# Kernel optimization log

Hardware: AMD Instinct MI355X
Metric: run time of the kernel (lower is better)

Reference implementation:

```python
import jax, jax.numpy as jnp
import numpy as np

B, L, D_MODEL = 2, 4096, 768
D_STATE, D_CONV, EXPAND = 16, 4, 2
D_INNER = EXPAND * D_MODEL
DT_RANK = -(-D_MODEL // 16)  # ceil(d_model/16) = 48


def _silu(x):
    return x * jax.nn.sigmoid(x)


def _dwconv(x, w, b):
    # x: (B, D_INNER, L); w: (D_INNER, K). Causal depthwise conv (torch pads both
    # sides with K-1 then slices [:L] == left-pad K-1, right-pad 0).
    y = jax.lax.conv_general_dilated(
        x, w[:, None, :], window_strides=(1,), padding=[(w.shape[-1] - 1, 0)],
        dimension_numbers=('NCH', 'OIH', 'NCH'), feature_group_count=x.shape[1])
    return y + b[None, :, None]


def _selective_scan(u, delta, A, Bm, Cm, Dv):
    # u, delta: (b,d,L); A: (d,n); Bm, Cm: (b,n,L); Dv: (d,)
    uT = jnp.moveaxis(u, -1, 0)      # (L,b,d)
    dT = jnp.moveaxis(delta, -1, 0)  # (L,b,d)
    BT = jnp.moveaxis(Bm, -1, 0)     # (L,b,n)
    CT = jnp.moveaxis(Cm, -1, 0)     # (L,b,n)

    def step(h, inp):
        u_t, d_t, B_t, C_t = inp
        dA = jnp.exp(d_t[..., None] * A)                       # (b,d,n)
        h = dA * h + (d_t * u_t)[..., None] * B_t[:, None, :]  # (b,d,n)
        y = jnp.einsum('bdn,bn->bd', h, C_t)
        return h, y

    h0 = jnp.zeros((u.shape[0], A.shape[0], A.shape[1]), u.dtype)
    _, ys = jax.lax.scan(step, h0, (uT, dT, BT, CT))
    y = jnp.moveaxis(ys, 0, -1)  # (b,d,L)
    return y + u * Dv[None, :, None]


def _branch(x, z, conv_w, conv_b, xproj_w, dtproj_w, dt_bias, A_log, Dv):
    x = _silu(_dwconv(x, conv_w, conv_b))
    dbl = jnp.einsum('bdl,ed->bel', x, xproj_w)  # e = DT_RANK + 2*D_STATE
    dt_low = dbl[:, :DT_RANK]
    Bm = dbl[:, DT_RANK:DT_RANK + D_STATE]
    Cm = dbl[:, DT_RANK + D_STATE:]
    dt = jnp.einsum('brl,dr->bdl', dt_low, dtproj_w)
    delta = jax.nn.softplus(dt + dt_bias[None, :, None])
    A = -jnp.exp(A_log)
    y = _selective_scan(x, delta, A, Bm, Cm, Dv)
    return y * _silu(z)


def _forward(hidden_states, in_proj_w, out_proj_w, conv_w_a, conv_b_a, conv_w_b,
             conv_b_b, x_proj_a_w, x_proj_b_w, dt_proj_a_w, dt_proj_b_w,
             dt_bias_a, dt_bias_b, A_a_log, A_b_log, D_a, D_b):
    xz = jnp.einsum('bld,ed->bel', hidden_states, in_proj_w)  # (B, 2*D_INNER, L)
    x_a, z_a = xz[:, :D_INNER], xz[:, D_INNER:]
    y_a = _branch(x_a, z_a, conv_w_a, conv_b_a, x_proj_a_w, dt_proj_a_w,
                  dt_bias_a, A_a_log, D_a)
    xz_b = xz[:, :, ::-1]  # flip sequence for backward direction
    x_b, z_b = xz_b[:, :D_INNER], xz_b[:, D_INNER:]
    y_b = _branch(x_b, z_b, conv_w_b, conv_b_b, x_proj_b_w, dt_proj_b_w,
                  dt_bias_b, A_b_log, D_b)
    y = y_a + y_b[:, :, ::-1]
    return jnp.einsum('bdl,od->blo', y, out_proj_w)  # (B, L, D_MODEL)


def setup_inputs() -> dict:
    key = jax.random.key(0)
    ks = jax.random.split(key, 10)
    s = 0.02
    rng = np.random.default_rng(0)
    # dt bias init: inverse-softplus of dt ~ LogUniform(1e-3, 1e-1)
    dt = np.exp(rng.uniform(size=D_INNER) * (np.log(0.1) - np.log(0.001))
                + np.log(0.001)).clip(min=1e-4)
    inv_dt = (dt + np.log(-np.expm1(-dt))).astype(np.float32)
    A_log = np.log(np.tile(np.arange(1, D_STATE + 1, dtype=np.float32),
                           (D_INNER, 1)))
    return {
        'hidden_states': jax.random.normal(ks[0], (B, L, D_MODEL), jnp.float32),
        'in_proj_w': s * jax.random.normal(ks[1], (2 * D_INNER, D_MODEL), jnp.float32),
        'out_proj_w': s * jax.random.normal(ks[2], (D_MODEL, D_INNER), jnp.float32),
        'conv_w_a': s * jax.random.normal(ks[3], (D_INNER, D_CONV), jnp.float32),
        'conv_b_a': jnp.zeros((D_INNER,), jnp.float32),
        'conv_w_b': s * jax.random.normal(ks[4], (D_INNER, D_CONV), jnp.float32),
        'conv_b_b': jnp.zeros((D_INNER,), jnp.float32),
        'x_proj_a_w': s * jax.random.normal(ks[5], (DT_RANK + 2 * D_STATE, D_INNER), jnp.float32),
        'x_proj_b_w': s * jax.random.normal(ks[6], (DT_RANK + 2 * D_STATE, D_INNER), jnp.float32),
        'dt_proj_a_w': (DT_RANK ** -0.5) * jax.random.uniform(ks[7], (D_INNER, DT_RANK), jnp.float32, -1.0, 1.0),
        'dt_proj_b_w': (DT_RANK ** -0.5) * jax.random.uniform(ks[8], (D_INNER, DT_RANK), jnp.float32, -1.0, 1.0),
        'dt_bias_a': jnp.asarray(inv_dt),
        'dt_bias_b': jnp.asarray(inv_dt),
        'A_a_log': jnp.asarray(A_log),
        'A_b_log': jnp.asarray(A_log),
        'D_a': jnp.ones((D_INNER,), jnp.float32),
        'D_b': jnp.ones((D_INNER,), jnp.float32),
    }


def reference(hidden_states, in_proj_w, out_proj_w, conv_w_a, conv_b_a, conv_w_b,
              conv_b_b, x_proj_a_w, x_proj_b_w, dt_proj_a_w, dt_proj_b_w,
              dt_bias_a, dt_bias_b, A_a_log, A_b_log, D_a, D_b):
    return _forward(hidden_states, in_proj_w, out_proj_w, conv_w_a, conv_b_a,
                    conv_w_b, conv_b_b, x_proj_a_w, x_proj_b_w, dt_proj_a_w,
                    dt_proj_b_w, dt_bias_a, dt_bias_b, A_a_log, A_b_log, D_a, D_b)
```

## Files before the change

### kernel.cpp

```cpp
#include <hip/hip_runtime.h>
#include <math.h>

#define BQ 2
#define LQ 4096
#define DM 768
#define DI 1536
#define DS 16
#define E80 80
#define NC 32
#define CH 128

typedef _Float16 half8 __attribute__((ext_vector_type(8)));
typedef _Float16 half4v __attribute__((ext_vector_type(4)));
typedef float f32x4 __attribute__((ext_vector_type(4)));

__device__ __forceinline__ ushort f2h_bits(float x) {
    return __builtin_bit_cast(ushort, (_Float16)x);
}

#define GLDS16(gsrc, ldst)                                                  \
    __builtin_amdgcn_global_load_lds(                                       \
        (const __attribute__((address_space(1))) void*)(gsrc),              \
        (__attribute__((address_space(3))) void*)(ldst), 16, 0, 0)

__global__ __launch_bounds__(256)
void pack_fp16(const float* __restrict__ src, _Float16* __restrict__ dst)
{
    long i = ((long)blockIdx.x * 256 + threadIdx.x) * 4;
    float4 v = *(const float4*)(src + i);
    half4v o = {(_Float16)v.x, (_Float16)v.y, (_Float16)v.z, (_Float16)v.w};
    *(half4v*)(dst + i) = o;
}

__global__ __launch_bounds__(256)
void pack_dtw(const float* __restrict__ dwa, const float* __restrict__ dwb,
              _Float16* __restrict__ dtw)
{
    int idx = blockIdx.x * 256 + threadIdx.x;
    int br = idx / DI, d = idx % DI;
    const float* W = (br ? dwb : dwa) + (long)d * 48;
    _Float16* o = dtw + (long)idx * 64;
#pragma unroll
    for (int k = 0; k < 48; k++) o[k] = (_Float16)W[k];
#pragma unroll
    for (int k = 48; k < 64; k++) o[k] = (_Float16)0.f;
}

template <typename CT>
__global__ __launch_bounds__(256, 4)
void gemm_mfma(const _Float16* __restrict__ Ah, const _Float16* __restrict__ Bh,
               CT* __restrict__ C, int K, int ldA, int ldB, int ldC,
               long strideA, long strideB, long strideC)
{
    __shared__ uint4 Af[2][16][64];
    __shared__ uint4 Bf[2][16][64];
    const int bz = blockIdx.z;
    const _Float16* Ab = Ah + (long)bz * strideA;
    const _Float16* Bb = Bh + (long)bz * strideB;
    CT* Cb = C + (long)bz * strideC;
    const int m0 = blockIdx.y * 128, n0 = blockIdx.x * 128;
    const int tid = threadIdx.x, w = tid >> 6, lane = tid & 63;
    const int mh = w & 1, nh = w >> 1;

    const _Float16* asrc[4];
    const _Float16* bsrc[4];
#pragma unroll
    for (int i = 0; i < 4; i++) {
        int f = w * 4 + i;
        int ks = f >> 3, t = f & 7;
        asrc[i] = Ab + (long)(m0 + t * 16 + (lane & 15)) * ldA + ks * 32 + (lane >> 4) * 8;
        bsrc[i] = Bb + (long)(n0 + t * 16 + (lane & 15)) * ldB + ks * 32 + (lane >> 4) * 8;
    }

    f32x4 acc[4][4];
#pragma unroll
    for (int i = 0; i < 4; i++)
#pragma unroll
        for (int j = 0; j < 4; j++) acc[i][j] = {0.f, 0.f, 0.f, 0.f};

    const int nt = K >> 6;

#pragma unroll
    for (int i = 0; i < 4; i++) {
        GLDS16(asrc[i], &Af[0][w * 4 + i][0]);
        GLDS16(bsrc[i], &Bf[0][w * 4 + i][0]);
        asrc[i] += 64; bsrc[i] += 64;
    }
    if (nt > 1) {
#pragma unroll
        for (int i = 0; i < 4; i++) {
            GLDS16(asrc[i], &Af[1][w * 4 + i][0]);
            GLDS16(bsrc[i], &Bf[1][w * 4 + i][0]);
            asrc[i] += 64; bsrc[i] += 64;
        }
    }

    for (int t = 0; t < nt; ++t) {
        const int cur = t & 1;
        if (t + 1 < nt)
            asm volatile("s_waitcnt vmcnt(8)" ::: "memory");
        else
            asm volatile("s_waitcnt vmcnt(0)" ::: "memory");
        __builtin_amdgcn_s_barrier();

#pragma unroll
        for (int ks = 0; ks < 2; ks++) {
            uint4 bu[4];
#pragma unroll
            for (int j = 0; j < 4; j++)
                bu[j] = Bf[cur][ks * 8 + nh * 4 + j][lane];
#pragma unroll
            for (int i = 0; i < 4; i++) {
                uint4 au = Af[cur][ks * 8 + mh * 4 + i][lane];
                half8 av = __builtin_bit_cast(half8, au);
#pragma unroll
                for (int j = 0; j < 4; j++) {
                    half8 bv = __builtin_bit_cast(half8, bu[j]);
                    acc[i][j] = __builtin_amdgcn_mfma_f32_16x16x32_f16(
                        av, bv, acc[i][j], 0, 0, 0);
                }
            }
        }
        __builtin_amdgcn_s_barrier();

        if (t + 2 < nt) {
#pragma unroll
            for (int i = 0; i < 4; i++) {
                GLDS16(asrc[i], &Af[cur][w * 4 + i][0]);
                GLDS16(bsrc[i], &Bf[cur][w * 4 + i][0]);
                asrc[i] += 64; bsrc[i] += 64;
            }
        }
    }

    const int r0 = (lane >> 4) * 4, cn = lane & 15;
#pragma unroll
    for (int i = 0; i < 4; i++) {
        int mrow = m0 + (mh * 4 + i) * 16 + r0;
#pragma unroll
        for (int j = 0; j < 4; j++) {
            int col = n0 + (nh * 4 + j) * 16 + cn;
#pragma unroll
            for (int r = 0; r < 4; r++)
                Cb[(long)(mrow + r) * ldC + col] = (CT)acc[i][j][r];
        }
    }
}

__global__ __launch_bounds__(256)
void conv_silu_t(const _Float16* __restrict__ xz,
                 const float* __restrict__ cwa, const float* __restrict__ cba,
                 const float* __restrict__ cwb, const float* __restrict__ cbb,
                 _Float16* __restrict__ ut)
{
    __shared__ float lraw[64][67];
    __shared__ float cu[64][72];
    __shared__ float lcw[64][5];
    const int l0 = blockIdx.x * 64, d0 = blockIdx.y * 64;
    const int z = blockIdx.z;
    const int br = z >> 1, b = z & 1;
    const _Float16* xb = xz + ((long)b * 2 * DI + d0) * LQ;
    const float* CW = br ? cwb : cwa;
    const float* CB = br ? cbb : cba;
    const int tid = threadIdx.x;

    {
        int dd = tid >> 2, k = tid & 3;
        lcw[dd][k] = CW[(d0 + dd) * 4 + k];
        if (tid < 64) lcw[tid][4] = CB[d0 + tid];
    }
    for (int i = tid; i < 64 * 67; i += 256) {
        int dd = i / 67, cc = i % 67;
        int src = l0 - 3 + cc;
        float v = 0.f;
        if (src >= 0)
            v = (float)xb[(long)dd * LQ + (br ? (LQ - 1 - src) : src)];
        lraw[dd][cc] = v;
    }
    __syncthreads();
#pragma unroll
    for (int q = 0; q < 16; q++) {
        int o = tid + q * 256;
        int dd = o & 63, ll = o >> 6;
        float a = lcw[dd][4];
        a = fmaf(lraw[dd][ll + 0], lcw[dd][0], a);
        a = fmaf(lraw[dd][ll + 1], lcw[dd][1], a);
        a = fmaf(lraw[dd][ll + 2], lcw[dd][2], a);
        a = fmaf(lraw[dd][ll + 3], lcw[dd][3], a);
        cu[ll][dd] = a * (1.f / (1.f + __expf(-a)));
    }
    __syncthreads();
    const int dg = (tid & 7) * 8;
#pragma unroll
    for (int p = 0; p < 2; p++) {
        int ll = (tid >> 3) + p * 32;
        float4 v0 = *(const float4*)&cu[ll][dg];
        float4 v1 = *(const float4*)&cu[ll][dg + 4];
        uint4 o;
        o.x = f2h_bits(v0.x) | ((unsigned)f2h_bits(v0.y) << 16);
        o.y = f2h_bits(v0.z) | ((unsigned)f2h_bits(v0.w) << 16);
        o.z = f2h_bits(v1.x) | ((unsigned)f2h_bits(v1.y) << 16);
        o.w = f2h_bits(v1.z) | ((unsigned)f2h_bits(v1.w) << 16);
        *(uint4*)(ut + ((long)z * LQ + l0 + ll) * DI + d0 + dg) = o;
    }
}

__global__ __launch_bounds__(256)
void xproj_mfma(const _Float16* __restrict__ ut, const _Float16* __restrict__ xpw,
                float* __restrict__ dbl)
{
    __shared__ uint4 Af[8][64];
    __shared__ uint4 Bf[10][64];
    const int m0 = blockIdx.x * 64;
    const int z = blockIdx.y;
    const _Float16* A = ut + (long)z * LQ * DI;
    const _Float16* W = xpw + (long)(z >> 1) * E80 * DI;
    float* out = dbl + (long)z * LQ * E80;
    const int tid = threadIdx.x, w = tid >> 6, lane = tid & 63;

    f32x4 acc[5];
#pragma unroll
    for (int j = 0; j < 5; j++) acc[j] = {0.f, 0.f, 0.f, 0.f};

    for (int k0 = 0; k0 < DI; k0 += 64) {
#pragma unroll
        for (int i = 0; i < 2; i++) {
            int f = w + i * 4;
            int row = m0 + (f & 3) * 16 + (lane & 15);
            int koff = k0 + (f >> 2) * 32 + (lane >> 4) * 8;
            Af[f][lane] = *(const uint4*)(A + (long)row * DI + koff);
        }
        for (int i = tid; i < 640; i += 256) {
            int f = i >> 6, ln = i & 63;
            int e = (f >> 1) * 16 + (ln & 15);
            int koff = k0 + (f & 1) * 32 + (ln >> 4) * 8;
            Bf[f][ln] = *(const uint4*)(W + (long)e * DI + koff);
        }
        __syncthreads();
#pragma unroll
        for (int ks = 0; ks < 2; ks++) {
            half8 av = __builtin_bit_cast(half8, Af[ks * 4 + w][lane]);
#pragma unroll
            for (int j = 0; j < 5; j++) {
                half8 bv = __builtin_bit_cast(half8, Bf[j * 2 + ks][lane]);
                acc[j] = __builtin_amdgcn_mfma_f32_16x16x32_f16(av, bv, acc[j], 0, 0, 0);
            }
        }
        __syncthreads();
    }
    const int r0 = (lane >> 4) * 4, cn = lane & 15;
    const int row = m0 + w * 16 + r0;
#pragma unroll
    for (int j = 0; j < 5; j++)
#pragma unroll
        for (int r = 0; r < 4; r++)
            out[(long)(row + r) * E80 + j * 16 + cn] = acc[j][r];
}

__global__ __launch_bounds__(256)
void delta_mfma(const float* __restrict__ dbl, const _Float16* __restrict__ dtw,
                const float* __restrict__ dba, const float* __restrict__ dbb,
                _Float16* __restrict__ dlt)
{
    __shared__ uint4 Af[8][64];
    __shared__ uint4 Bf[16][64];
    const int m0 = blockIdx.x * 64;
    const int n0 = blockIdx.y * 128;
    const int z  = blockIdx.z;
    const float* bias = (z >> 1) ? dbb : dba;
    const float* Ab = dbl + (long)z * LQ * E80;
    const _Float16* Wb = dtw + (long)(z >> 1) * DI * 64;
    _Float16* ob = dlt + (long)z * LQ * DI;
    const int tid = threadIdx.x, w = tid >> 6, lane = tid & 63;

#pragma unroll
    for (int i = 0; i < 2; i++) {
        int s = tid + i * 256;
        int f = s >> 6, ln = s & 63;
        int mt = f >> 1, ks = f & 1;
        int row = m0 + mt * 16 + (ln & 15);
        int koff = ks * 32 + (ln >> 4) * 8;
        uint4 o = {0u, 0u, 0u, 0u};
        if (koff < 48) {
            const float* p = Ab + (long)row * E80 + koff;
            float4 v0 = *(const float4*)p;
            float4 v1 = *(const float4*)(p + 4);
            o.x = f2h_bits(v0.x) | ((unsigned)f2h_bits(v0.y) << 16);
            o.y = f2h_bits(v0.z) | ((unsigned)f2h_bits(v0.w) << 16);
            o.z = f2h_bits(v1.x) | ((unsigned)f2h_bits(v1.y) << 16);
            o.w = f2h_bits(v1.z) | ((unsigned)f2h_bits(v1.w) << 16);
        }
        Af[f][ln] = o;
    }
#pragma unroll
    for (int i = 0; i < 4; i++) {
        int s = tid + i * 256;
        int f = s >> 6, ln = s & 63;
        int nt = f >> 1, ks = f & 1;
        int d = n0 + nt * 16 + (ln & 15);
        int koff = ks * 32 + (ln >> 4) * 8;
        Bf[f][ln] = *(const uint4*)(Wb + (long)d * 64 + koff);
    }
    __syncthreads();

    f32x4 acc[8];
#pragma unroll
    for (int j = 0; j < 8; j++) acc[j] = {0.f, 0.f, 0.f, 0.f};
#pragma unroll
    for (int ks = 0; ks < 2; ks++) {
        half8 av = __builtin_bit_cast(half8, Af[w * 2 + ks][lane]);
#pragma unroll
        for (int j = 0; j < 8; j++) {
            half8 bv = __builtin_bit_cast(half8, Bf[j * 2 + ks][lane]);
            acc[j] = __builtin_amdgcn_mfma_f32_16x16x32_f16(av, bv, acc[j], 0, 0, 0);
        }
    }
    const int r0 = (lane >> 4) * 4, cn = lane & 15;
    const int row = m0 + w * 16 + r0;
#pragma unroll
    for (int j = 0; j < 8; j++) {
        int d = n0 + j * 16 + cn;
        float bi = bias[d];
#pragma unroll
        for (int r = 0; r < 4; r++) {
            float a = acc[j][r] + bi;
            float sp = (a > 20.f) ? a : __logf(1.f + __expf(a));
            ob[(long)(row + r) * DI + d] = (_Float16)sp;
        }
    }
}

__global__ __launch_bounds__(256)
void transpose_z(const _Float16* __restrict__ xz, _Float16* __restrict__ zt)
{
    __shared__ float t[64][65];
    const int l0 = blockIdx.x * 64, d0 = blockIdx.y * 64, b = blockIdx.z;
    const _Float16* src = xz + ((long)b * 2 * DI + DI + d0) * LQ + l0;
    const int tid = threadIdx.x;
#pragma unroll
    for (int p = 0; p < 2; p++) {
        int g = tid + p * 256;
        int dd = g >> 3, c8 = (g & 7) * 8;
        half8 v = *(const half8*)&src[(long)dd * LQ + c8];
#pragma unroll
        for (int j = 0; j < 8; j++) t[c8 + j][dd] = (float)v[j];
    }
    __syncthreads();
    const int l = tid >> 2, seg = (tid & 3) * 16;
    ushort tmp[16];
#pragma unroll
    for (int j = 0; j < 16; j++) tmp[j] = f2h_bits(t[l][seg + j]);
    uint4 p0, p1;
    p0.x = tmp[0] | (tmp[1] << 16);  p0.y = tmp[2] | (tmp[3] << 16);
    p0.z = tmp[4] | (tmp[5] << 16);  p0.w = tmp[6] | (tmp[7] << 16);
    p1.x = tmp[8] | (tmp[9] << 16);  p1.y = tmp[10] | (tmp[11] << 16);
    p1.z = tmp[12] | (tmp[13] << 16); p1.w = tmp[14] | (tmp[15] << 16);
    ushort* dst = (ushort*)(zt + ((long)b * LQ + l0 + l) * DI + d0 + seg);
    *(uint4*)dst = p0;
    *(uint4*)(dst + 8) = p1;
}

__global__ __launch_bounds__(256)
void scan_p1(const _Float16* __restrict__ ut, const _Float16* __restrict__ dlt,
             const float* __restrict__ dbl,
             const float* __restrict__ Ala, const float* __restrict__ Alb,
             float* __restrict__ Sdl, float* __restrict__ Hloc)
{
    const int d = blockIdx.x * 256 + threadIdx.x;
    const int c = blockIdx.y;
    const int z = blockIdx.z;
    const int br = z >> 1;
    const float* Al = br ? Alb : Ala;
    float An[16];
#pragma unroll
    for (int i = 0; i < 4; i++) {
        float4 v = *(const float4*)&Al[(long)d * 16 + i * 4];
        An[i * 4] = -__expf(v.x); An[i * 4 + 1] = -__expf(v.y);
        An[i * 4 + 2] = -__expf(v.z); An[i * 4 + 3] = -__expf(v.w);
    }
    bool fast = true;
#pragma unroll
    for (int n = 0; n < 16; n++)
        fast = fast && (__builtin_fabsf(An[n] + (float)(n + 1)) < 1e-3f);

    const long lbase = (long)z * LQ + (long)c * CH;
    const _Float16* ub = ut + lbase * DI + d;
    const _Float16* db = dlt + lbase * DI + d;
    const float* bc = dbl + lbase * E80 + 48;

    float h[16];
#pragma unroll
    for (int n = 0; n < 16; n++) h[n] = 0.f;
    float sdl = 0.f;

    for (int t0 = 0; t0 < CH; t0 += 8) {
        _Float16 uu[8], dd[8];
#pragma unroll
        for (int j = 0; j < 8; j++) {
            uu[j] = ub[(long)(t0 + j) * DI];
            dd[j] = db[(long)(t0 + j) * DI];
        }
#pragma unroll
        for (int j = 0; j < 8; j++) {
            float dl = (float)dd[j];
            float u  = (float)uu[j];
            sdl += dl;
            float du = dl * u;
            const float* Bp = bc + (long)(t0 + j) * E80;
            float Bv[16];
#pragma unroll
            for (int i = 0; i < 4; i++) {
                float4 v = *(const float4*)&Bp[i * 4];
                Bv[i * 4] = v.x; Bv[i * 4 + 1] = v.y;
                Bv[i * 4 + 2] = v.z; Bv[i * 4 + 3] = v.w;
            }
            if (fast) {
                float r = __expf(-dl);
                float p = r;
                h[0] = fmaf(p, h[0], du * Bv[0]);
#pragma unroll
                for (int n = 1; n < 16; n++) {
                    p *= r;
                    h[n] = fmaf(p, h[n], du * Bv[n]);
                }
            } else {
#pragma unroll
                for (int n = 0; n < 16; n++)
                    h[n] = fmaf(__expf(dl * An[n]), h[n], du * Bv[n]);
            }
        }
    }
    Sdl[((long)z * NC + c) * DI + d] = sdl;
    float* Hp = Hloc + (((long)z * NC + c) * DI + d) * 16;
#pragma unroll
    for (int i = 0; i < 4; i++)
        *(float4*)&Hp[i * 4] = make_float4(h[i * 4], h[i * 4 + 1], h[i * 4 + 2], h[i * 4 + 3]);
}

__global__ __launch_bounds__(256)
void scan_p2(const float* __restrict__ Sdl, const float* __restrict__ Hloc,
             const float* __restrict__ Ala, const float* __restrict__ Alb,
             float* __restrict__ h0)
{
    const int idx = blockIdx.x * 256 + threadIdx.x;
    const int z = blockIdx.y;
    const int d = idx >> 4, n = idx & 15;
    const float* Al = (z >> 1) ? Alb : Ala;
    const float An = -__expf(Al[(long)d * 16 + n]);
    float h = 0.f;
    for (int c = 0; c < NC; c++) {
        h0[((long)z * NC + c) * DI * 16 + idx] = h;
        float sdl = Sdl[((long)z * NC + c) * DI + d];
        float Hl = Hloc[((long)z * NC + c) * DI * 16 + idx];
        h = fmaf(__expf(An * sdl), h, Hl);
    }
}

__global__ __launch_bounds__(256)
void scan_p3(const _Float16* __restrict__ ut, const _Float16* __restrict__ dlt,
             const float* __restrict__ dbl, const float* __restrict__ h0,
             const float* __restrict__ Ala, const float* __restrict__ Alb,
             const float* __restrict__ Da, const float* __restrict__ Db,
             _Float16* __restrict__ ya, _Float16* __restrict__ yb)
{
    const int d = blockIdx.x * 256 + threadIdx.x;
    const int c = blockIdx.y;
    const int z = blockIdx.z;
    const int br = z >> 1, b = z & 1;
    const float* Al = br ? Alb : Ala;
    float An[16];
#pragma unroll
    for (int i = 0; i < 4; i++) {
        float4 v = *(const float4*)&Al[(long)d * 16 + i * 4];
        An[i * 4] = -__expf(v.x); An[i * 4 + 1] = -__expf(v.y);
        An[i * 4 + 2] = -__expf(v.z); An[i * 4 + 3] = -__expf(v.w);
    }
    bool fast = true;
#pragma unroll
    for (int n = 0; n < 16; n++)
        fast = fast && (__builtin_fabsf(An[n] + (float)(n + 1)) < 1e-3f);

    const float Dd = (br ? Db : Da)[d];
    const long lbase = (long)z * LQ + (long)c * CH;
    const _Float16* ub = ut + lbase * DI + d;
    const _Float16* db = dlt + lbase * DI + d;
    const float* bc = dbl + lbase * E80 + 48;
    const float* Hp = h0 + (((long)z * NC + c) * DI + d) * 16;
    float h[16];
#pragma unroll
    for (int i = 0; i < 4; i++) {
        float4 v = *(const float4*)&Hp[i * 4];
        h[i * 4] = v.x; h[i * 4 + 1] = v.y; h[i * 4 + 2] = v.z; h[i * 4 + 3] = v.w;
    }
    _Float16* yo = br ? yb : ya;

    for (int t0 = 0; t0 < CH; t0 += 8) {
        _Float16 uu[8], dd[8];
#pragma unroll
        for (int j = 0; j < 8; j++) {
            uu[j] = ub[(long)(t0 + j) * DI];
            dd[j] = db[(long)(t0 + j) * DI];
        }
#pragma unroll
        for (int j = 0; j < 8; j++) {
            float dl = (float)dd[j];
            float u  = (float)uu[j];
            float du = dl * u;
            const float* Bp = bc + (long)(t0 + j) * E80;
            float Bv[16], Cv[16];
#pragma unroll
            for (int i = 0; i < 4; i++) {
                float4 v = *(const float4*)&Bp[i * 4];
                Bv[i * 4] = v.x; Bv[i * 4 + 1] = v.y;
                Bv[i * 4 + 2] = v.z; Bv[i * 4 + 3] = v.w;
                float4 w2 = *(const float4*)&Bp[16 + i * 4];
                Cv[i * 4] = w2.x; Cv[i * 4 + 1] = w2.y;
                Cv[i * 4 + 2] = w2.z; Cv[i * 4 + 3] = w2.w;
            }
            float y = u * Dd;
            if (fast) {
                float r = __expf(-dl);
                float p = r;
                h[0] = fmaf(p, h[0], du * Bv[0]);
                y = fmaf(h[0], Cv[0], y);
#pragma unroll
                for (int n = 1; n < 16; n++) {
                    p *= r;
                    h[n] = fmaf(p, h[n], du * Bv[n]);
                    y = fmaf(h[n], Cv[n], y);
                }
            } else {
#pragma unroll
                for (int n = 0; n < 16; n++) {
                    h[n] = fmaf(__expf(dl * An[n]), h[n], du * Bv[n]);
                    y = fmaf(h[n], Cv[n], y);
                }
            }
            int t = c * CH + t0 + j;
            long lorig = br ? (LQ - 1 - t) : t;
            yo[((long)b * LQ + lorig) * DI + d] = (_Float16)y;
        }
    }
}

__global__ __launch_bounds__(256)
void fuse_y(const _Float16* __restrict__ ya, const _Float16* __restrict__ yb,
            const _Float16* __restrict__ zt, _Float16* __restrict__ yf)
{
    long i = ((long)blockIdx.x * 256 + threadIdx.x) * 8;
    half8 a = *(const half8*)(ya + i);
    half8 b = *(const half8*)(yb + i);
    half8 zz = *(const half8*)(zt + i);
    half8 o;
#pragma unroll
    for (int j = 0; j < 8; j++) {
        float y = (float)a[j] + (float)b[j];
        float zv = (float)zz[j];
        o[j] = (_Float16)(y * (zv / (1.f + __expf(-zv))));
    }
    *(half8*)(yf + i) = o;
}

extern "C" void kernel_launch(void* const* d_in, const int* in_sizes, int n_in,
                              void* d_out, int out_size, void* d_ws, size_t ws_size,
                              hipStream_t stream)
{
    const float* hs  = (const float*)d_in[0];
    const float* Wi  = (const float*)d_in[1];
    const float* Wo  = (const float*)d_in[2];
    const float* cwa = (const float*)d_in[3];
    const float* cba = (const float*)d_in[4];
    const float* cwb = (const float*)d_in[5];
    const float* cbb = (const float*)d_in[6];
    const float* xpa = (const float*)d_in[7];
    const float* xpb = (const float*)d_in[8];
    const float* dwa = (const float*)d_in[9];
    const float* dwb = (const float*)d_in[10];
    const float* dba = (const float*)d_in[11];
    const float* dbb = (const float*)d_in[12];
    const float* Ala = (const float*)d_in[13];
    const float* Alb = (const float*)d_in[14];
    const float* Da  = (const float*)d_in[15];
    const float* Db  = (const float*)d_in[16];
    float* out = (float*)d_out;

    float* ws = (float*)d_ws;
    _Float16* xz   = (_Float16*)ws;
    _Float16* dl_t = (_Float16*)ws;
    _Float16* ya   = (_Float16*)(ws + 12582912);
    _Float16* yb   = (_Float16*)(ws + 18874368);
    float*    dbl  = ws + 25165824;
    _Float16* u_t  = (_Float16*)(ws + 26476544);
    _Float16* yf   = (_Float16*)(ws + 26476544);
    _Float16* z_t  = (_Float16*)(ws + 39059456);
    float*    Sdl  = ws + 45350912;
    float*    Hloc = ws + 45547520;
    float*    h0   = ws + 48693248;
    _Float16* hsb  = (_Float16*)(ws + 45350912);
    _Float16* Wib  = (_Float16*)(ws + 48496640);
    _Float16* xpw  = (_Float16*)(ws + 49676288);
    _Float16* dtw  = (_Float16*)(ws + 49799168);
    _Float16* Wob  = (_Float16*)(ws + 45350912);

    pack_fp16<<<6144, 256, 0, stream>>>(hs, hsb);
    pack_fp16<<<2304, 256, 0, stream>>>(Wi, Wib);
    pack_fp16<<<120, 256, 0, stream>>>(xpa, xpw);
    pack_fp16<<<120, 256, 0, stream>>>(xpb, xpw + 122880);
    pack_dtw<<<12, 256, 0, stream>>>(dwa, dwb, dtw);
    gemm_mfma<_Float16><<<dim3(32, 24, 2), 256, 0, stream>>>(
        Wib, hsb, xz, DM, DM, DM, LQ,
        0L, (long)LQ * DM, (long)2 * DI * LQ);
    conv_silu_t<<<dim3(64, 24, 4), 256, 0, stream>>>(xz, cwa, cba, cwb, cbb, u_t);
    xproj_mfma<<<dim3(64, 4), 256, 0, stream>>>(u_t, xpw, dbl);
    transpose_z<<<dim3(64, 24, 2), 256, 0, stream>>>(xz, z_t);
    delta_mfma<<<dim3(64, 12, 4), 256, 0, stream>>>(dbl, dtw, dba, dbb, dl_t);
    scan_p1<<<dim3(6, NC, 4), 256, 0, stream>>>(u_t, dl_t, dbl, Ala, Alb, Sdl, Hloc);
    scan_p2<<<dim3(96, 4), 256, 0, stream>>>(Sdl, Hloc, Ala, Alb, h0);
    scan_p3<<<dim3(6, NC, 4), 256, 0, stream>>>(u_t, dl_t, dbl, h0, Ala, Alb, Da, Db, ya, yb);
    pack_fp16<<<1152, 256, 0, stream>>>(Wo, Wob);
    fuse_y<<<6144, 256, 0, stream>>>(ya, yb, z_t, yf);
    gemm_mfma<float><<<dim3(6, 32, 2), 256, 0, stream>>>(
        yf, Wob, out, DI, DI, DI, DM,
        (long)LQ * DI, 0L, (long)LQ * DM);
}
```

Measured before the change: 551.2 us.

## Split-K the x_proj and out_proj GEMMs with atomic accumulation

Partitions the K dimension of the x_proj GEMM into four chunks and of the output projection GEMM into two, launching more blocks and accumulating partial results with float atomicAdd. Output buffers are zeroed with memsets beforehand. The aim is to fill more compute units on GEMMs whose grids were small (256 and 384 blocks). In exchange it adds atomic traffic, two memset operations and non-deterministic summation order.

```diff
diff --git a/kernel.cpp b/kernel.cpp
--- a/kernel.cpp
+++ b/kernel.cpp
@@ -46,18 +46,19 @@
     for (int k = 48; k < 64; k++) o[k] = (_Float16)0.f;
 }
 
-template <typename CT>
+template <typename CT, bool ATOMIC>
 __global__ __launch_bounds__(256, 4)
 void gemm_mfma(const _Float16* __restrict__ Ah, const _Float16* __restrict__ Bh,
                CT* __restrict__ C, int K, int ldA, int ldB, int ldC,
-               long strideA, long strideB, long strideC)
+               long strideA, long strideB, long strideC, int nbz, int koff)
 {
     __shared__ uint4 Af[2][16][64];
     __shared__ uint4 Bf[2][16][64];
     const int bz = blockIdx.z;
-    const _Float16* Ab = Ah + (long)bz * strideA;
-    const _Float16* Bb = Bh + (long)bz * strideB;
-    CT* Cb = C + (long)bz * strideC;
+    const int batch = bz % nbz, kh = bz / nbz;
+    const _Float16* Ab = Ah + (long)batch * strideA + (long)kh * koff;
+    const _Float16* Bb = Bh + (long)batch * strideB + (long)kh * koff;
+    CT* Cb = C + (long)batch * strideC;
     const int m0 = blockIdx.y * 128, n0 = blockIdx.x * 128;
     const int tid = threadIdx.x, w = tid >> 6, lane = tid & 63;
     const int mh = w & 1, nh = w >> 1;
@@ -141,8 +142,12 @@
         for (int j = 0; j < 4; j++) {
             int col = n0 + (nh * 4 + j) * 16 + cn;
 #pragma unroll
-            for (int r = 0; r < 4; r++)
-                Cb[(long)(mrow + r) * ldC + col] = (CT)acc[i][j][r];
+            for (int r = 0; r < 4; r++) {
+                if constexpr (ATOMIC)
+                    atomicAdd(&Cb[(long)(mrow + r) * ldC + col], acc[i][j][r]);
+                else
+                    Cb[(long)(mrow + r) * ldC + col] = (CT)acc[i][j][r];
+            }
         }
     }
 }
@@ -213,6 +218,7 @@
     __shared__ uint4 Bf[10][64];
     const int m0 = blockIdx.x * 64;
     const int z = blockIdx.y;
+    const int kh = blockIdx.z;
     const _Float16* A = ut + (long)z * LQ * DI;
     const _Float16* W = xpw + (long)(z >> 1) * E80 * DI;
     float* out = dbl + (long)z * LQ * E80;
@@ -222,7 +228,7 @@
 #pragma unroll
     for (int j = 0; j < 5; j++) acc[j] = {0.f, 0.f, 0.f, 0.f};
 
-    for (int k0 = 0; k0 < DI; k0 += 64) {
+    for (int k0 = kh * 384; k0 < (kh + 1) * 384; k0 += 64) {
 #pragma unroll
         for (int i = 0; i < 2; i++) {
             int f = w + i * 4;
@@ -254,7 +260,7 @@
     for (int j = 0; j < 5; j++)
 #pragma unroll
         for (int r = 0; r < 4; r++)
-            out[(long)(row + r) * E80 + j * 16 + cn] = acc[j][r];
+            atomicAdd(&out[(long)(row + r) * E80 + j * 16 + cn], acc[j][r]);
 }
 
 __global__ __launch_bounds__(256)
@@ -602,16 +608,18 @@
     _Float16* dtw  = (_Float16*)(ws + 49799168);
     _Float16* Wob  = (_Float16*)(ws + 45350912);
 
+    hipMemsetAsync(dbl, 0, (size_t)4 * LQ * E80 * sizeof(float), stream);
+    hipMemsetAsync(out, 0, (size_t)out_size, stream);
     pack_fp16<<<6144, 256, 0, stream>>>(hs, hsb);
     pack_fp16<<<2304, 256, 0, stream>>>(Wi, Wib);
     pack_fp16<<<120, 256, 0, stream>>>(xpa, xpw);
     pack_fp16<<<120, 256, 0, stream>>>(xpb, xpw + 122880);
     pack_dtw<<<12, 256, 0, stream>>>(dwa, dwb, dtw);
-    gemm_mfma<_Float16><<<dim3(32, 24, 2), 256, 0, stream>>>(
+    gemm_mfma<_Float16, false><<<dim3(32, 24, 2), 256, 0, stream>>>(
         Wib, hsb, xz, DM, DM, DM, LQ,
-        0L, (long)LQ * DM, (long)2 * DI * LQ);
+        0L, (long)LQ * DM, (long)2 * DI * LQ, 2, 0);
     conv_silu_t<<<dim3(64, 24, 4), 256, 0, stream>>>(xz, cwa, cba, cwb, cbb, u_t);
-    xproj_mfma<<<dim3(64, 4), 256, 0, stream>>>(u_t, xpw, dbl);
+    xproj_mfma<<<dim3(64, 4, 4), 256, 0, stream>>>(u_t, xpw, dbl);
     transpose_z<<<dim3(64, 24, 2), 256, 0, stream>>>(xz, z_t);
     delta_mfma<<<dim3(64, 12, 4), 256, 0, stream>>>(dbl, dtw, dba, dbb, dl_t);
     scan_p1<<<dim3(6, NC, 4), 256, 0, stream>>>(u_t, dl_t, dbl, Ala, Alb, Sdl, Hloc);
@@ -619,7 +627,7 @@
     scan_p3<<<dim3(6, NC, 4), 256, 0, stream>>>(u_t, dl_t, dbl, h0, Ala, Alb, Da, Db, ya, yb);
     pack_fp16<<<1152, 256, 0, stream>>>(Wo, Wob);
     fuse_y<<<6144, 256, 0, stream>>>(ya, yb, z_t, yf);
-    gemm_mfma<float><<<dim3(6, 32, 2), 256, 0, stream>>>(
-        yf, Wob, out, DI, DI, DI, DM,
-        (long)LQ * DI, 0L, (long)LQ * DM);
-}
+    gemm_mfma<float, true><<<dim3(6, 32, 4), 256, 0, stream>>>(
+        yf, Wob, out, 768, DI, DI, DM,
+        (long)LQ * DI, 0L, (long)LQ * DM, 2, 768);
+}
```

Result: slower. 565.8 us (+2.6%).
